# Optimization experiments

Hardware: AMD Instinct MI355X
Metric: run time of the kernel (lower is better)

## Reference

```python
import jax, jax.numpy as jnp
import numpy as np

B, S, E = 2, 2048, 2048
A, H = 2048, 16  # attention_dim, n_heads
HD = A // H      # head_dim = 128
ROPE_THETA = 10000.0


def setup_inputs() -> dict:
    key = jax.random.key(0)
    k1, k2, k3 = jax.random.split(key, 3)
    x = jax.random.normal(k1, (B, S, E), dtype=jnp.float32)
    W_qkv = jax.random.normal(k2, (E, 3 * A), dtype=jnp.float32) * 0.02
    W_out = jax.random.normal(k3, (A, E), dtype=jnp.float32) * 0.02
    return {"x": x, "W_qkv": W_qkv, "W_out": W_out}


def _apply_rope(x):
    # x: (B, H, S, D); interleaved rotary pairs (rotary-embedding-torch default)
    b, h, s, d = x.shape
    inv_freq = 1.0 / (ROPE_THETA ** (jnp.arange(0, d, 2, dtype=jnp.float32) / d))
    freqs = jnp.arange(s, dtype=jnp.float32)[:, None] * inv_freq[None, :]  # (S, D/2)
    cos, sin = jnp.cos(freqs), jnp.sin(freqs)
    xr = x.reshape(b, h, s, d // 2, 2)
    x1, x2 = xr[..., 0], xr[..., 1]
    o1 = x1 * cos - x2 * sin
    o2 = x1 * sin + x2 * cos
    return jnp.stack([o1, o2], axis=-1).reshape(b, h, s, d)


def reference(x, W_qkv, W_out):
    b, s, _ = x.shape
    qkv = (x @ W_qkv).reshape(b, s, 3, H, HD)          # (B,S,3,H,hd)
    qkv = jnp.moveaxis(qkv, 3, 1)                      # movedim(-2,1) -> (B,H,S,3,hd)
    q, k, v = qkv[..., 0, :], qkv[..., 1, :], qkv[..., 2, :]
    q = _apply_rope(q)
    k = _apply_rope(k)
    scale = 1.0 / jnp.sqrt(jnp.asarray(HD, dtype=x.dtype))
    scores = jnp.einsum("bhqd,bhkd->bhqk", q, k) * scale
    attn = jax.nn.softmax(scores, axis=-1)
    out = jnp.einsum("bhqk,bhkd->bhqd", attn, v)       # (B,H,S,hd)
    out = out.transpose(0, 2, 1, 3).reshape(b, s, A)   # (B,S,A)
    return out @ W_out
```

## Files before the change

### kernel.cpp

```cpp
#include <hip/hip_runtime.h>
#include <math.h>

typedef float  f32x4 __attribute__((ext_vector_type(4)));
typedef short  s16x8 __attribute__((ext_vector_type(8)));
typedef short  s16x4 __attribute__((ext_vector_type(4)));
typedef unsigned short u16;
typedef unsigned int u32;

static __device__ __forceinline__ u16 f32_to_bf16_rne(float f) {
    u32 u = __builtin_bit_cast(u32, f);
    u32 r = u + 0x7fffu + ((u >> 16) & 1u);
    return (u16)(r >> 16);
}
static __device__ __forceinline__ u32 pack_bf16_rhu(float a, float b) {
    u32 ua = __builtin_bit_cast(u32, a);
    u32 ub = __builtin_bit_cast(u32, b);
    return ((ua + 0x8000u) >> 16) | ((ub + 0x8000u) & 0xffff0000u);
}
static __device__ __forceinline__ float bf16_to_f32(u16 h) {
    return __builtin_bit_cast(float, (u32)h << 16);
}

static __device__ __forceinline__ void gl2lds16(const void* g, void* l) {
    __builtin_amdgcn_global_load_lds(
        (const __attribute__((address_space(1))) u32*)g,
        (__attribute__((address_space(3))) u32*)l, 16, 0, 0);
}

__global__ __launch_bounds__(256) void k_cast(const float* __restrict__ in,
                                              u16* __restrict__ out) {
    int i = (blockIdx.x * 256 + threadIdx.x) * 8;
    float4 a = *reinterpret_cast<const float4*>(in + i);
    float4 b = *reinterpret_cast<const float4*>(in + i + 4);
    s16x8 o;
    o[0] = (short)f32_to_bf16_rne(a.x); o[1] = (short)f32_to_bf16_rne(a.y);
    o[2] = (short)f32_to_bf16_rne(a.z); o[3] = (short)f32_to_bf16_rne(a.w);
    o[4] = (short)f32_to_bf16_rne(b.x); o[5] = (short)f32_to_bf16_rne(b.y);
    o[6] = (short)f32_to_bf16_rne(b.z); o[7] = (short)f32_to_bf16_rne(b.w);
    *reinterpret_cast<s16x8*>(out + i) = o;
}

__global__ __launch_bounds__(256) void k_transpose_cast(const float* __restrict__ in,
                                                        u16* __restrict__ out,
                                                        int R, int C) {
    __shared__ float TT[64 * 130];
    const int t = threadIdx.x;
    const int ct = blockIdx.x, rt = blockIdx.y;
    const int tr = t >> 4;
    const int tc = t & 15;
    float4 v[8];
#pragma unroll
    for (int u = 0; u < 8; ++u) {
        int r = u * 16 + tr;
        v[u] = *reinterpret_cast<const float4*>(in + (size_t)(rt * 128 + r) * C + ct * 64 + tc * 4);
    }
#pragma unroll
    for (int u = 0; u < 8; ++u) {
        int r = u * 16 + tr;
        TT[(tc * 4 + 0) * 130 + r] = v[u].x;
        TT[(tc * 4 + 1) * 130 + r] = v[u].y;
        TT[(tc * 4 + 2) * 130 + r] = v[u].z;
        TT[(tc * 4 + 3) * 130 + r] = v[u].w;
    }
    __syncthreads();
#pragma unroll
    for (int u = 0; u < 4; ++u) {
        int oc = u * 16 + tr;
        int r0 = tc * 8;
        s16x8 o;
#pragma unroll
        for (int e = 0; e < 8; ++e)
            o[e] = (short)f32_to_bf16_rne(TT[oc * 130 + r0 + e]);
        *reinterpret_cast<s16x8*>(out + (size_t)(ct * 64 + oc) * R + rt * 128 + r0) = o;
    }
}

template<bool BF16OUT, bool ROPE>
__global__ __launch_bounds__(256) void k_gemm_bt(const u16* __restrict__ Amat,
                                                 const u16* __restrict__ Bt,
                                                 void* __restrict__ Cout,
                                                 int M, int N, int K) {
    __shared__ __align__(16) u16 As[128 * 64];
    __shared__ __align__(16) u16 Bs[128 * 64];
    const int t = threadIdx.x;
    const int lane = t & 63, wave = t >> 6;
    const int m16 = lane & 15, qd = lane >> 4;
    const int wm = (wave >> 1) * 64, wn = (wave & 1) * 64;
    const size_t m0 = (size_t)blockIdx.y * 128, n0 = (size_t)blockIdx.x * 128;
    const int srow = lane >> 3;
    const int schunk = (lane & 7) ^ srow;

    f32x4 acc[4][4] = {};

    for (int k0 = 0; k0 < K; k0 += 64) {
#pragma unroll
        for (int j = 0; j < 4; ++j) {
            int rbase = j * 32 + wave * 8;
            int r = rbase + srow;
            gl2lds16(Amat + (m0 + r) * (size_t)K + k0 + schunk * 8, &As[rbase * 64]);
            gl2lds16(Bt   + (n0 + r) * (size_t)K + k0 + schunk * 8, &Bs[rbase * 64]);
        }
        __syncthreads();
#pragma unroll
        for (int kh = 0; kh < 2; ++kh) {
            s16x8 af[4], bf[4];
#pragma unroll
            for (int i = 0; i < 4; ++i) {
                int ra = wm + i * 16 + m16;
                int pa = (kh * 4 + qd) ^ (ra & 7);
                af[i] = *reinterpret_cast<const s16x8*>(&As[ra * 64 + pa * 8]);
                int rb = wn + i * 16 + m16;
                int pb = (kh * 4 + qd) ^ (rb & 7);
                bf[i] = *reinterpret_cast<const s16x8*>(&Bs[rb * 64 + pb * 8]);
            }
#pragma unroll
            for (int i = 0; i < 4; ++i)
#pragma unroll
                for (int jj = 0; jj < 4; ++jj)
                    acc[i][jj] = __builtin_amdgcn_mfma_f32_16x16x32_bf16(af[i], bf[jj], acc[i][jj], 0, 0, 0);
        }
        __syncthreads();
    }
    if (ROPE && n0 < 4096) {
        float invf[4];
#pragma unroll
        for (int j = 0; j < 4; ++j) {
            int pi = ((int)(wn + j * 16 + m16) & 127) >> 1;
            invf[j] = __expf(-0.14391156831f * (float)pi);
        }
#pragma unroll
        for (int i = 0; i < 4; ++i)
#pragma unroll
            for (int j = 0; j < 4; ++j)
#pragma unroll
                for (int r = 0; r < 4; ++r) {
                    float v = acc[i][j][r];
                    float p = __shfl_xor(v, 1);
                    size_t row = m0 + wm + i * 16 + qd * 4 + r;
                    float f = (float)(int)(row & 2047) * invf[j];
                    float sn, cs;
                    __sincosf(f, &sn, &cs);
                    float res = (m16 & 1) ? fmaf(p, sn, v * cs) : fmaf(v, cs, -p * sn);
                    size_t col = n0 + wn + j * 16 + m16;
                    ((u16*)Cout)[row * N + col] = f32_to_bf16_rne(res);
                }
    } else {
#pragma unroll
        for (int i = 0; i < 4; ++i)
#pragma unroll
            for (int j = 0; j < 4; ++j)
#pragma unroll
                for (int r = 0; r < 4; ++r) {
                    size_t row = m0 + wm + i * 16 + qd * 4 + r;
                    size_t col = n0 + wn + j * 16 + m16;
                    if (BF16OUT)
                        ((u16*)Cout)[row * N + col] = f32_to_bf16_rne(acc[i][j][r]);
                    else
                        ((float*)Cout)[row * N + col] = acc[i][j][r];
                }
    }
}

template<bool BF16OUT, bool ROPE>
__global__ __launch_bounds__(512, 2) void k_gemm384(const u16* __restrict__ Amat,
                                                    const u16* __restrict__ Bt,
                                                    void* __restrict__ Cout,
                                                    int M, int N, int K) {
    __shared__ __align__(16) u16 As[2][128 * 64];
    __shared__ __align__(16) u16 Bs[2][384 * 64];
    const int t = threadIdx.x;
    const int lane = t & 63, wave = t >> 6;
    const int m16 = lane & 15, qd = lane >> 4;
    const int wr = wave >> 2, wc = wave & 3;
    const int srow = lane >> 3;
    const int sch = (lane & 7) ^ srow;

    int bx, by;
    if (gridDim.x == 16 && gridDim.y == 32) {
        int orig = blockIdx.y * gridDim.x + blockIdx.x;
        int xcd = orig & 7, loc = orig >> 3;
        int cx = xcd & 3, cy = xcd >> 2;
        bx = cx * 4 + (loc & 3);
        by = cy * 16 + (loc >> 2);
    } else {
        bx = blockIdx.x; by = blockIdx.y;
    }
    const size_t m0 = (size_t)by * 128, n0 = (size_t)bx * 384;

    const u16* Ab = Amat + m0 * (size_t)K;
    const u16* Bb = Bt + n0 * (size_t)K;
    const int NT = K >> 6;

    auto stage128 = [&](const u16* gbase, u16* lbase, int k0) {
        int rb0 = wave * 8;
        gl2lds16(gbase + (size_t)(rb0 + srow) * K + k0 + sch * 8, lbase + rb0 * 64);
        int rb1 = rb0 + 64;
        gl2lds16(gbase + (size_t)(rb1 + srow) * K + k0 + sch * 8, lbase + rb1 * 64);
    };

    f32x4 acc[4][6] = {};
    s16x8 af[4][2], bq[6][2];

    stage128(Bb,            &Bs[0][0],        0);
    stage128(Bb + 128 * (size_t)K, &Bs[0][128 * 64], 0);
    stage128(Bb + 256 * (size_t)K, &Bs[0][256 * 64], 0);
    stage128(Ab,            &As[0][0],        0);
    if (NT > 1) {
        stage128(Bb,            &Bs[1][0],        64);
        stage128(Bb + 128 * (size_t)K, &Bs[1][128 * 64], 64);
        asm volatile("s_waitcnt vmcnt(4)" ::: "memory");
    } else {
        asm volatile("s_waitcnt vmcnt(0)" ::: "memory");
    }
    __builtin_amdgcn_s_barrier();

    for (int kt = 0; kt < NT; ++kt) {
        const int p = kt & 1;

#pragma unroll
        for (int i = 0; i < 4; ++i) {
            int ra = wr * 64 + i * 16 + m16;
            af[i][0] = *reinterpret_cast<const s16x8*>(&As[p][ra * 64 + ((qd)     ^ (ra & 7)) * 8]);
        }
#pragma unroll
        for (int j = 0; j < 6; ++j) {
            int rb = wc * 96 + j * 16 + m16;
            bq[j][0] = *reinterpret_cast<const s16x8*>(&Bs[p][rb * 64 + ((qd)     ^ (rb & 7)) * 8]);
        }
        if (kt + 1 < NT) stage128(Bb + 256 * (size_t)K, &Bs[p ^ 1][256 * 64], (kt + 1) << 6);
#pragma unroll
        for (int i = 0; i < 4; ++i) {
            int ra = wr * 64 + i * 16 + m16;
            af[i][1] = *reinterpret_cast<const s16x8*>(&As[p][ra * 64 + ((4 + qd) ^ (ra & 7)) * 8]);
        }
#pragma unroll
        for (int j = 0; j < 6; ++j) {
            int rb = wc * 96 + j * 16 + m16;
            bq[j][1] = *reinterpret_cast<const s16x8*>(&Bs[p][rb * 64 + ((4 + qd) ^ (rb & 7)) * 8]);
        }
        if (kt + 1 < NT) stage128(Ab, &As[p ^ 1][0], (kt + 1) << 6);

        __builtin_amdgcn_s_setprio(1);
#pragma unroll
        for (int i = 0; i < 4; ++i)
#pragma unroll
            for (int j = 0; j < 6; ++j)
                acc[i][j] = __builtin_amdgcn_mfma_f32_16x16x32_bf16(af[i][0], bq[j][0], acc[i][j], 0, 0, 0);
        __builtin_amdgcn_s_setprio(0);

        asm volatile("s_waitcnt lgkmcnt(0)" ::: "memory");
        __builtin_amdgcn_s_barrier();

        if (kt + 2 < NT) {
            stage128(Bb,            &Bs[p][0],        (kt + 2) << 6);
            stage128(Bb + 128 * (size_t)K, &Bs[p][128 * 64], (kt + 2) << 6);
        }
        __builtin_amdgcn_s_setprio(1);
#pragma unroll
        for (int i = 0; i < 4; ++i)
#pragma unroll
            for (int j = 0; j < 6; ++j)
                acc[i][j] = __builtin_amdgcn_mfma_f32_16x16x32_bf16(af[i][1], bq[j][1], acc[i][j], 0, 0, 0);
        __builtin_amdgcn_s_setprio(0);
        if (kt + 2 < NT) {
            asm volatile("s_waitcnt vmcnt(4)" ::: "memory");
        } else {
            asm volatile("s_waitcnt vmcnt(0)" ::: "memory");
        }
        __builtin_amdgcn_s_barrier();
    }

    if (ROPE) {
        float invf[6];
#pragma unroll
        for (int j = 0; j < 6; ++j) {
            int pi = ((int)(n0 + wc * 96 + j * 16 + m16) & 127) >> 1;
            invf[j] = __expf(-0.14391156831f * (float)pi);
        }
#pragma unroll
        for (int i = 0; i < 4; ++i)
#pragma unroll
            for (int j = 0; j < 6; ++j) {
                size_t colbase = n0 + wc * 96 + j * 16;
                if (colbase < 4096) {
#pragma unroll
                    for (int r = 0; r < 4; ++r) {
                        float v = acc[i][j][r];
                        float pv = __shfl_xor(v, 1);
                        size_t row = m0 + wr * 64 + i * 16 + qd * 4 + r;
                        float f = (float)(int)(row & 2047) * invf[j];
                        float sn, cs;
                        __sincosf(f, &sn, &cs);
                        float res = (m16 & 1) ? fmaf(pv, sn, v * cs) : fmaf(v, cs, -pv * sn);
                        ((u16*)Cout)[row * N + colbase + m16] = f32_to_bf16_rne(res);
                    }
                } else {
#pragma unroll
                    for (int r = 0; r < 4; ++r) {
                        size_t row = m0 + wr * 64 + i * 16 + qd * 4 + r;
                        ((u16*)Cout)[row * N + colbase + m16] = f32_to_bf16_rne(acc[i][j][r]);
                    }
                }
            }
    } else {
#pragma unroll
        for (int i = 0; i < 4; ++i)
#pragma unroll
            for (int j = 0; j < 6; ++j)
#pragma unroll
                for (int r = 0; r < 4; ++r) {
                    size_t row = m0 + wr * 64 + i * 16 + qd * 4 + r;
                    size_t col = n0 + wc * 96 + j * 16 + m16;
                    if (BF16OUT)
                        ((u16*)Cout)[row * N + col] = f32_to_bf16_rne(acc[i][j][r]);
                    else
                        ((float*)Cout)[row * N + col] = acc[i][j][r];
                }
    }
}

__global__ __launch_bounds__(256) void k_transpose_v(const u16* __restrict__ qkv,
                                                     u16* __restrict__ vt) {
    __shared__ u16 TT[128 * 130];
    const int t = threadIdx.x;
    const int st = blockIdx.x;
    const int bh = blockIdx.y;
    const int b = bh >> 4, h = bh & 15;
    const u16* src = qkv + (size_t)b * 2048 * 6144 + 4096 + (size_t)h * 128;
    const int tr = t >> 4, tc = t & 15;
    s16x8 v[8];
#pragma unroll
    for (int u = 0; u < 8; ++u) {
        int s = u * 16 + tr;
        v[u] = *reinterpret_cast<const s16x8*>(src + (size_t)(st * 128 + s) * 6144 + tc * 8);
    }
#pragma unroll
    for (int u = 0; u < 8; ++u) {
        int s = u * 16 + tr;
#pragma unroll
        for (int e = 0; e < 8; ++e)
            TT[(tc * 8 + e) * 130 + s] = (u16)v[u][e];
    }
    __syncthreads();
    u16* dst = vt + (size_t)bh * 128 * 2048 + st * 128;
#pragma unroll
    for (int u = 0; u < 8; ++u) {
        int d = u * 16 + tr;
        int s0 = tc * 8;
        s16x8 o;
#pragma unroll
        for (int e = 0; e < 8; ++e) o[e] = (short)TT[d * 130 + s0 + e];
        *reinterpret_cast<s16x8*>(dst + (size_t)d * 2048 + s0) = o;
    }
}

__global__ __launch_bounds__(512, 4) void k_flash(const u16* __restrict__ qkv,
                                                  const u16* __restrict__ vt,
                                                  u16* __restrict__ out) {
    __shared__ __align__(16) u16 KS[128 * 136];
    __shared__ __align__(16) u16 VS[128 * 136];
    const int t = threadIdx.x, lane = t & 63, wave = t >> 6;
    const int m16 = lane & 15, qd = lane >> 4;
    const int bh = blockIdx.y, b = bh >> 4, h = bh & 15;
    const int q0 = blockIdx.x * 128;
    const u16* Qg = qkv + (size_t)b * 2048 * 6144 + (size_t)h * 128;
    const u16* Kg = Qg + 2048;
    const u16* Vtg = vt + (size_t)bh * 128 * 2048;
    const float C2 = 0.12751743f;

    int srow[4], scol[4], pi0[4];
#pragma unroll
    for (int ci = 0; ci < 4; ++ci) {
        int idx = ci * 512 + t;
        int row = idx >> 4, c = idx & 15;
        srow[ci] = row;
        scol[ci] = c * 8;
        pi0[ci] = 32 * (c >> 2) + 16 * (c & 1) + 4 * ((c >> 1) & 1);
    }

    s16x8 qf[4];
#pragma unroll
    for (int kc = 0; kc < 4; ++kc)
        qf[kc] = *reinterpret_cast<const s16x8*>(
            Qg + (size_t)(q0 + wave * 16 + m16) * 6144 + kc * 32 + qd * 8);

    f32x4 accO[8] = {};
    float mrow = -1e30f, lrow = 0.f;

    for (int kt = 0; kt < 16; ++kt) {
        const int s0 = kt * 128;
        s16x8 kreg[4], vreg[4];
#pragma unroll
        for (int ci = 0; ci < 4; ++ci) {
            kreg[ci] = *reinterpret_cast<const s16x8*>(
                Kg + (size_t)(s0 + srow[ci]) * 6144 + scol[ci]);
            vreg[ci] = *reinterpret_cast<const s16x8*>(
                Vtg + (size_t)srow[ci] * 2048 + s0 + scol[ci]);
        }
        __syncthreads();
#pragma unroll
        for (int ci = 0; ci < 4; ++ci) {
            *reinterpret_cast<s16x8*>(&KS[srow[ci] * 136 + scol[ci]]) = kreg[ci];
            s16x4 lo = __builtin_shufflevector(vreg[ci], vreg[ci], 0, 1, 2, 3);
            s16x4 hi = __builtin_shufflevector(vreg[ci], vreg[ci], 4, 5, 6, 7);
            *reinterpret_cast<s16x4*>(&VS[srow[ci] * 136 + pi0[ci]]) = lo;
            *reinterpret_cast<s16x4*>(&VS[srow[ci] * 136 + pi0[ci] + 8]) = hi;
        }
        __syncthreads();

        f32x4 accS[8] = {};
#pragma unroll
        for (int kc = 0; kc < 4; ++kc)
#pragma unroll
            for (int nj = 0; nj < 8; ++nj) {
                s16x8 kf = *reinterpret_cast<const s16x8*>(
                    &KS[(nj * 16 + m16) * 136 + (kc * 4 + qd) * 8]);
                accS[nj] = __builtin_amdgcn_mfma_f32_16x16x32_bf16(kf, qf[kc], accS[nj], 0, 0, 0);
            }

        float mx = accS[0][0];
#pragma unroll
        for (int nj = 0; nj < 8; ++nj)
#pragma unroll
            for (int r = 0; r < 4; ++r) mx = fmaxf(mx, accS[nj][r]);
        mx *= C2;
        mx = fmaxf(mx, __shfl_xor(mx, 16));
        mx = fmaxf(mx, __shfl_xor(mx, 32));
        float mn = fmaxf(mrow, mx);
        float alpha = __builtin_amdgcn_exp2f(mrow - mn);
        mrow = mn;
        float ls = 0.f;
        s16x4 pk[8];
#pragma unroll
        for (int nj = 0; nj < 8; ++nj) {
            float p0 = __builtin_amdgcn_exp2f(fmaf(accS[nj][0], C2, -mn));
            float p1 = __builtin_amdgcn_exp2f(fmaf(accS[nj][1], C2, -mn));
            float p2 = __builtin_amdgcn_exp2f(fmaf(accS[nj][2], C2, -mn));
            float p3 = __builtin_amdgcn_exp2f(fmaf(accS[nj][3], C2, -mn));
            ls += (p0 + p1) + (p2 + p3);
            u32 lo = pack_bf16_rhu(p0, p1);
            u32 hi = pack_bf16_rhu(p2, p3);
            uint2 pr = make_uint2(lo, hi);
            pk[nj] = __builtin_bit_cast(s16x4, pr);
        }
        ls += __shfl_xor(ls, 16);
        ls += __shfl_xor(ls, 32);
        lrow = lrow * alpha + ls;
        float aO[4];
#pragma unroll
        for (int r = 0; r < 4; ++r) aO[r] = __shfl(alpha, qd * 4 + r);
#pragma unroll
        for (int dj = 0; dj < 8; ++dj)
#pragma unroll
            for (int r = 0; r < 4; ++r) accO[dj][r] *= aO[r];

#pragma unroll
        for (int kb = 0; kb < 4; ++kb) {
            s16x8 af = __builtin_shufflevector(pk[2 * kb], pk[2 * kb + 1],
                                               0, 1, 2, 3, 4, 5, 6, 7);
#pragma unroll
            for (int dj = 0; dj < 8; ++dj) {
                s16x8 vf = *reinterpret_cast<const s16x8*>(
                    &VS[(dj * 16 + m16) * 136 + kb * 32 + qd * 8]);
                accO[dj] = __builtin_amdgcn_mfma_f32_16x16x32_bf16(af, vf, accO[dj], 0, 0, 0);
            }
        }
    }
    float invl = 1.0f / lrow;
    float iv[4];
#pragma unroll
    for (int r = 0; r < 4; ++r) iv[r] = __shfl(invl, qd * 4 + r);
#pragma unroll
    for (int r = 0; r < 4; ++r) {
        size_t row = (size_t)b * 2048 + q0 + wave * 16 + qd * 4 + r;
#pragma unroll
        for (int dj = 0; dj < 8; ++dj)
            out[row * 2048 + h * 128 + dj * 16 + m16] =
                f32_to_bf16_rne(accO[dj][r] * iv[r]);
    }
}

extern "C" void kernel_launch(void* const* d_in, const int* in_sizes, int n_in,
                              void* d_out, int out_size, void* d_ws, size_t ws_size,
                              hipStream_t stream) {
    const float* x     = (const float*)d_in[0];
    const float* W_qkv = (const float*)d_in[1];
    const float* W_out = (const float*)d_in[2];
    float* out = (float*)d_out;

    char* ws = (char*)d_ws;
    u16* xb   = (u16*)(ws);
    u16* Wqt  = (u16*)(ws + (16u << 20));
    u16* Wot  = (u16*)(ws + (40u << 20));
    u16* qkvb = (u16*)(ws + (48u << 20));
    u16* attn = (u16*)(ws + (96u << 20));
    u16* vtg  = (u16*)(ws + (112u << 20));

    k_cast<<<4096, 256, 0, stream>>>(x, xb);
    k_transpose_cast<<<dim3(96, 16), 256, 0, stream>>>(W_qkv, Wqt, 2048, 6144);
    k_transpose_cast<<<dim3(32, 16), 256, 0, stream>>>(W_out, Wot, 2048, 2048);
    k_gemm384<true, true><<<dim3(16, 32), 512, 0, stream>>>(xb, Wqt, qkvb, 4096, 6144, 2048);
    k_transpose_v<<<dim3(16, 32), 256, 0, stream>>>(qkvb, vtg);
    k_flash<<<dim3(16, 32), 512, 0, stream>>>(qkvb, vtg, attn);
    k_gemm_bt<false, false><<<dim3(16, 32), 256, 0, stream>>>(attn, Wot, out, 4096, 2048, 2048);
}
```

Baseline: 401.8 us.

## Replace output projection GEMM with double-buffered 128x256 pipelined kernel

The simple single-buffered 128x128 output-projection GEMM is replaced by a new 512-thread kernel with 128x256 tiles, double-buffered LDS staging split across the two k-halves, raised MFMA priority, and an XCD-aware block remap. The aim is to overlap global-to-LDS loads with MFMA work and to improve L2 locality and operand reuse for the final GEMM. The old kernel is deleted. The trade-off is fewer blocks (256) on the device and more LDS per block.

```diff
diff --git a/kernel.cpp b/kernel.cpp
--- a/kernel.cpp
+++ b/kernel.cpp
@@ -1,7 +1,7 @@
 #include <hip/hip_runtime.h>
 #include <math.h>
 
-typedef float  f32x4 __attribute__((ext_vector_type(4)));
+typedef float  f32x4  __attribute__((ext_vector_type(4)));
 typedef short  s16x8 __attribute__((ext_vector_type(8)));
 typedef short  s16x4 __attribute__((ext_vector_type(4)));
 typedef unsigned short u16;
@@ -72,92 +72,6 @@
         for (int e = 0; e < 8; ++e)
             o[e] = (short)f32_to_bf16_rne(TT[oc * 130 + r0 + e]);
         *reinterpret_cast<s16x8*>(out + (size_t)(ct * 64 + oc) * R + rt * 128 + r0) = o;
-    }
-}
-
-template<bool BF16OUT, bool ROPE>
-__global__ __launch_bounds__(256) void k_gemm_bt(const u16* __restrict__ Amat,
-                                                 const u16* __restrict__ Bt,
-                                                 void* __restrict__ Cout,
-                                                 int M, int N, int K) {
-    __shared__ __align__(16) u16 As[128 * 64];
-    __shared__ __align__(16) u16 Bs[128 * 64];
-    const int t = threadIdx.x;
-    const int lane = t & 63, wave = t >> 6;
-    const int m16 = lane & 15, qd = lane >> 4;
-    const int wm = (wave >> 1) * 64, wn = (wave & 1) * 64;
-    const size_t m0 = (size_t)blockIdx.y * 128, n0 = (size_t)blockIdx.x * 128;
-    const int srow = lane >> 3;
-    const int schunk = (lane & 7) ^ srow;
-
-    f32x4 acc[4][4] = {};
-
-    for (int k0 = 0; k0 < K; k0 += 64) {
-#pragma unroll
-        for (int j = 0; j < 4; ++j) {
-            int rbase = j * 32 + wave * 8;
-            int r = rbase + srow;
-            gl2lds16(Amat + (m0 + r) * (size_t)K + k0 + schunk * 8, &As[rbase * 64]);
-            gl2lds16(Bt   + (n0 + r) * (size_t)K + k0 + schunk * 8, &Bs[rbase * 64]);
-        }
-        __syncthreads();
-#pragma unroll
-        for (int kh = 0; kh < 2; ++kh) {
-            s16x8 af[4], bf[4];
-#pragma unroll
-            for (int i = 0; i < 4; ++i) {
-                int ra = wm + i * 16 + m16;
-                int pa = (kh * 4 + qd) ^ (ra & 7);
-                af[i] = *reinterpret_cast<const s16x8*>(&As[ra * 64 + pa * 8]);
-                int rb = wn + i * 16 + m16;
-                int pb = (kh * 4 + qd) ^ (rb & 7);
-                bf[i] = *reinterpret_cast<const s16x8*>(&Bs[rb * 64 + pb * 8]);
-            }
-#pragma unroll
-            for (int i = 0; i < 4; ++i)
-#pragma unroll
-                for (int jj = 0; jj < 4; ++jj)
-                    acc[i][jj] = __builtin_amdgcn_mfma_f32_16x16x32_bf16(af[i], bf[jj], acc[i][jj], 0, 0, 0);
-        }
-        __syncthreads();
-    }
-    if (ROPE && n0 < 4096) {
-        float invf[4];
-#pragma unroll
-        for (int j = 0; j < 4; ++j) {
-            int pi = ((int)(wn + j * 16 + m16) & 127) >> 1;
-            invf[j] = __expf(-0.14391156831f * (float)pi);
-        }
-#pragma unroll
-        for (int i = 0; i < 4; ++i)
-#pragma unroll
-            for (int j = 0; j < 4; ++j)
-#pragma unroll
-                for (int r = 0; r < 4; ++r) {
-                    float v = acc[i][j][r];
-                    float p = __shfl_xor(v, 1);
-                    size_t row = m0 + wm + i * 16 + qd * 4 + r;
-                    float f = (float)(int)(row & 2047) * invf[j];
-                    float sn, cs;
-                    __sincosf(f, &sn, &cs);
-                    float res = (m16 & 1) ? fmaf(p, sn, v * cs) : fmaf(v, cs, -p * sn);
-                    size_t col = n0 + wn + j * 16 + m16;
-                    ((u16*)Cout)[row * N + col] = f32_to_bf16_rne(res);
-                }
-    } else {
-#pragma unroll
-        for (int i = 0; i < 4; ++i)
-#pragma unroll
-            for (int j = 0; j < 4; ++j)
-#pragma unroll
-                for (int r = 0; r < 4; ++r) {
-                    size_t row = m0 + wm + i * 16 + qd * 4 + r;
-                    size_t col = n0 + wn + j * 16 + m16;
-                    if (BF16OUT)
-                        ((u16*)Cout)[row * N + col] = f32_to_bf16_rne(acc[i][j][r]);
-                    else
-                        ((float*)Cout)[row * N + col] = acc[i][j][r];
-                }
     }
 }
 
@@ -201,12 +115,12 @@
     f32x4 acc[4][6] = {};
     s16x8 af[4][2], bq[6][2];
 
-    stage128(Bb,            &Bs[0][0],        0);
+    stage128(Bb,                   &Bs[0][0],        0);
     stage128(Bb + 128 * (size_t)K, &Bs[0][128 * 64], 0);
     stage128(Bb + 256 * (size_t)K, &Bs[0][256 * 64], 0);
-    stage128(Ab,            &As[0][0],        0);
+    stage128(Ab,                   &As[0][0],        0);
     if (NT > 1) {
-        stage128(Bb,            &Bs[1][0],        64);
+        stage128(Bb,                   &Bs[1][0],        64);
         stage128(Bb + 128 * (size_t)K, &Bs[1][128 * 64], 64);
         asm volatile("s_waitcnt vmcnt(4)" ::: "memory");
     } else {
@@ -252,7 +166,7 @@
         __builtin_amdgcn_s_barrier();
 
         if (kt + 2 < NT) {
-            stage128(Bb,            &Bs[p][0],        (kt + 2) << 6);
+            stage128(Bb,                   &Bs[p][0],        (kt + 2) << 6);
             stage128(Bb + 128 * (size_t)K, &Bs[p][128 * 64], (kt + 2) << 6);
         }
         __builtin_amdgcn_s_setprio(1);
@@ -317,6 +231,124 @@
                         ((float*)Cout)[row * N + col] = acc[i][j][r];
                 }
     }
+}
+
+__global__ __launch_bounds__(512, 2) void k_gemmo(const u16* __restrict__ Amat,
+                                                  const u16* __restrict__ Bt,
+                                                  float* __restrict__ Cout,
+                                                  int M, int N, int K) {
+    __shared__ __align__(16) u16 As[2][128 * 64];
+    __shared__ __align__(16) u16 Bs[2][256 * 64];
+    const int t = threadIdx.x;
+    const int lane = t & 63, wave = t >> 6;
+    const int m16 = lane & 15, qd = lane >> 4;
+    const int wr = wave >> 2, wc = wave & 3;
+    const int srow = lane >> 3;
+    const int sch = (lane & 7) ^ srow;
+
+    int bx, by;
+    if (gridDim.x == 8 && gridDim.y == 32) {
+        int orig = blockIdx.y * gridDim.x + blockIdx.x;
+        int xcd = orig & 7, loc = orig >> 3;
+        int cx = xcd & 1, cy = xcd >> 1;
+        bx = cx * 4 + (loc & 3);
+        by = cy * 8 + (loc >> 2);
+    } else {
+        bx = blockIdx.x; by = blockIdx.y;
+    }
+    const size_t m0 = (size_t)by * 128, n0 = (size_t)bx * 256;
+
+    const u16* Ab = Amat + m0 * (size_t)K;
+    const u16* Bb = Bt + n0 * (size_t)K;
+    const int NT = K >> 6;
+
+    auto stage128 = [&](const u16* gbase, u16* lbase, int k0) {
+        int rb0 = wave * 8;
+        gl2lds16(gbase + (size_t)(rb0 + srow) * K + k0 + sch * 8, lbase + rb0 * 64);
+        int rb1 = rb0 + 64;
+        gl2lds16(gbase + (size_t)(rb1 + srow) * K + k0 + sch * 8, lbase + rb1 * 64);
+    };
+
+    f32x4 acc[4][4] = {};
+    s16x8 af[4][2], bq[4][2];
+
+    stage128(Ab,                   &As[0][0],        0);
+    stage128(Bb,                   &Bs[0][0],        0);
+    stage128(Bb + 128 * (size_t)K, &Bs[0][128 * 64], 0);
+    if (NT > 1) {
+        stage128(Ab,               &As[1][0],        64);
+        stage128(Bb,               &Bs[1][0],        64);
+        asm volatile("s_waitcnt vmcnt(4)" ::: "memory");
+    } else {
+        asm volatile("s_waitcnt vmcnt(0)" ::: "memory");
+    }
+    __builtin_amdgcn_s_barrier();
+
+    for (int kt = 0; kt < NT; ++kt) {
+        const int p = kt & 1;
+
+#pragma unroll
+        for (int i = 0; i < 4; ++i) {
+            int ra = wr * 64 + i * 16 + m16;
+            af[i][0] = *reinterpret_cast<const s16x8*>(&As[p][ra * 64 + ((qd)     ^ (ra & 7)) * 8]);
+        }
+#pragma unroll
+        for (int j = 0; j < 4; ++j) {
+            int rb = wc * 64 + j * 16 + m16;
+            bq[j][0] = *reinterpret_cast<const s16x8*>(&Bs[p][rb * 64 + ((qd)     ^ (rb & 7)) * 8]);
+        }
+        if (kt + 1 < NT) stage128(Bb + 128 * (size_t)K, &Bs[p ^ 1][128 * 64], (kt + 1) << 6);
+#pragma unroll
+        for (int i = 0; i < 4; ++i) {
+            int ra = wr * 64 + i * 16 + m16;
+            af[i][1] = *reinterpret_cast<const s16x8*>(&As[p][ra * 64 + ((4 + qd) ^ (ra & 7)) * 8]);
+        }
+#pragma unroll
+        for (int j = 0; j < 4; ++j) {
+            int rb = wc * 64 + j * 16 + m16;
+            bq[j][1] = *reinterpret_cast<const s16x8*>(&Bs[p][rb * 64 + ((4 + qd) ^ (rb & 7)) * 8]);
+        }
+
+        __builtin_amdgcn_s_setprio(1);
+#pragma unroll
+        for (int i = 0; i < 4; ++i)
+#pragma unroll
+            for (int j = 0; j < 4; ++j)
+                acc[i][j] = __builtin_amdgcn_mfma_f32_16x16x32_bf16(af[i][0], bq[j][0], acc[i][j], 0, 0, 0);
+        __builtin_amdgcn_s_setprio(0);
+
+        asm volatile("s_waitcnt lgkmcnt(0)" ::: "memory");
+        __builtin_amdgcn_s_barrier();
+
+        if (kt + 2 < NT) {
+            stage128(Ab, &As[p][0], (kt + 2) << 6);
+            stage128(Bb, &Bs[p][0], (kt + 2) << 6);
+        }
+        __builtin_amdgcn_s_setprio(1);
+#pragma unroll
+        for (int i = 0; i < 4; ++i)
+#pragma unroll
+            for (int j = 0; j < 4; ++j)
+                acc[i][j] = __builtin_amdgcn_mfma_f32_16x16x32_bf16(af[i][1], bq[j][1], acc[i][j], 0, 0, 0);
+        __builtin_amdgcn_s_setprio(0);
+        if (kt + 2 < NT) {
+            asm volatile("s_waitcnt vmcnt(4)" ::: "memory");
+        } else {
+            asm volatile("s_waitcnt vmcnt(0)" ::: "memory");
+        }
+        __builtin_amdgcn_s_barrier();
+    }
+
+#pragma unroll
+    for (int i = 0; i < 4; ++i)
+#pragma unroll
+        for (int j = 0; j < 4; ++j)
+#pragma unroll
+            for (int r = 0; r < 4; ++r) {
+                size_t row = m0 + wr * 64 + i * 16 + qd * 4 + r;
+                size_t col = n0 + wc * 64 + j * 16 + m16;
+                Cout[row * N + col] = acc[i][j][r];
+            }
 }
 
 __global__ __launch_bounds__(256) void k_transpose_v(const u16* __restrict__ qkv,
@@ -502,5 +534,5 @@
     k_gemm384<true, true><<<dim3(16, 32), 512, 0, stream>>>(xb, Wqt, qkvb, 4096, 6144, 2048);
     k_transpose_v<<<dim3(16, 32), 256, 0, stream>>>(qkvb, vtg);
     k_flash<<<dim3(16, 32), 512, 0, stream>>>(qkvb, vtg, attn);
-    k_gemm_bt<false, false><<<dim3(16, 32), 256, 0, stream>>>(attn, Wot, out, 4096, 2048, 2048);
-}
+    k_gemmo<<<dim3(8, 32), 512, 0, stream>>>(attn, Wot, out, 4096, 2048, 2048);
+}
```

After: 400.5 us. No clear change (-0.3%).
